# Kernel optimization log

Measured on AMD Instinct MI355X. Metric: run time of the kernel, lower is better.

## Reference

```python
import jax, jax.numpy as jnp
import numpy as np

N = 50000
E_RAND = 800000
F_IN = 128
H = 4          # num_heads
D_HID = 32     # hidden per-head dim
D_OUT = 32     # output per-head dim
NEG_SLOPE_ATTN = 0.2   # DGL GATConv attention leaky_relu
NEG_SLOPE_ACT = 0.01   # F.leaky_relu default activation


def setup_inputs() -> dict:
    key = jax.random.key(0)
    ks = jax.random.split(key, 12)
    x = jax.random.normal(ks[0], (N, F_IN), dtype=jnp.float32)
    src_r = jax.random.randint(ks[1], (E_RAND,), 0, N, dtype=jnp.int32)
    dst_r = jax.random.randint(ks[2], (E_RAND,), 0, N, dtype=jnp.int32)
    loop = jnp.arange(N, dtype=jnp.int32)
    src = jnp.concatenate([src_r, loop])  # add_self_loop
    dst = jnp.concatenate([dst_r, loop])
    sc1 = 1.0 / np.sqrt(F_IN)
    sc2 = 1.0 / np.sqrt(H * D_HID)
    W1 = jax.random.normal(ks[3], (F_IN, H * D_HID), dtype=jnp.float32) * sc1
    al1 = jax.random.normal(ks[4], (H, D_HID), dtype=jnp.float32) * sc1
    ar1 = jax.random.normal(ks[5], (H, D_HID), dtype=jnp.float32) * sc1
    b1 = jnp.zeros((H * D_HID,), dtype=jnp.float32)
    W2 = jax.random.normal(ks[6], (H * D_HID, H * D_OUT), dtype=jnp.float32) * sc2
    al2 = jax.random.normal(ks[7], (H, D_OUT), dtype=jnp.float32) * sc2
    ar2 = jax.random.normal(ks[8], (H, D_OUT), dtype=jnp.float32) * sc2
    b2 = jnp.zeros((H * D_OUT,), dtype=jnp.float32)
    return {"x": x, "src": src, "dst": dst,
            "W1": W1, "al1": al1, "ar1": ar1, "b1": b1,
            "W2": W2, "al2": al2, "ar2": ar2, "b2": b2}


def gat_conv(x, src, dst, W, al, ar, b, act_slope):
    n = x.shape[0]
    h, d = al.shape
    feat = (x @ W).reshape(n, h, d)                 # [N,H,D]
    el = jnp.einsum('nhd,hd->nh', feat, al)         # [N,H]
    er = jnp.einsum('nhd,hd->nh', feat, ar)
    # edge attention score on edge u->v: leaky_relu(el[u] + er[v])
    e = jax.nn.leaky_relu(el[src] + er[dst], NEG_SLOPE_ATTN)  # [E,H]
    # edge softmax over incoming edges of each dst node (self-loops guarantee >=1 edge)
    m = jax.ops.segment_max(e, dst, num_segments=n)           # [N,H]
    ex = jnp.exp(e - m[dst])
    s = jax.ops.segment_sum(ex, dst, num_segments=n)
    a = ex / s[dst]                                           # [E,H]
    # attention-weighted scatter-sum of source features
    out = jax.ops.segment_sum(a[:, :, None] * feat[src], dst, num_segments=n)  # [N,H,D]
    out = out + b.reshape(h, d)
    if act_slope is not None:
        out = jax.nn.leaky_relu(out, act_slope)
    return out.reshape(n, h * d)                    # flatten(1)


def reference(x, src, dst, W1, al1, ar1, b1, W2, al2, ar2, b2):
    h = gat_conv(x, src, dst, W1, al1, ar1, b1, NEG_SLOPE_ACT)
    out = gat_conv(h, src, dst, W2, al2, ar2, b2, None)  # last layer: no activation
    return out
```

## Files before the change

### kernel.cpp

```cpp
#include <hip/hip_runtime.h>
#include <hip/hip_bf16.h>
#include <hip/hip_fp16.h>

#define HEADS 4
#define DHEAD 32
#define FDIM 128
#define BCAP 64
#define RPB 64
#define BINSH 8
#define MAXBINS 256
#define NREP 4
#define WSTRIDE 68

__device__ __forceinline__ void stage_W(const float* __restrict__ W, float* Ws) {
    const float4* Wg = (const float4*)W;
    float4* Wl = (float4*)Ws;
    for (int i = threadIdx.x; i < FDIM * FDIM / 4; i += 256)
        Wl[i] = Wg[i];
}

__device__ __forceinline__ void gemm_core(
    const float* __restrict__ X, const float* __restrict__ al,
    const float* __restrict__ ar, __half* __restrict__ feat,
    float* __restrict__ el, float* __restrict__ er, int n, const float* Ws) {
    int head = __builtin_amdgcn_readfirstlane(threadIdx.x >> 6);
    int lane = threadIdx.x & 63;
    int row = blockIdx.x * RPB + lane;
    bool valid = row < n;
    int cr = valid ? row : (n - 1);
    const float4* xp = (const float4*)(X + (size_t)cr * FDIM);

    const float* wb = Ws + head * DHEAD;

    float acc[32];
#pragma unroll
    for (int j = 0; j < 32; j++) acc[j] = 0.f;

    float4 a = xp[0];
    for (int k4 = 0; k4 < FDIM / 4; k4++) {
        float4 an = (k4 < FDIM / 4 - 1) ? xp[k4 + 1] : a;
#pragma unroll
        for (int kk = 0; kk < 4; kk++) {
            const float4* wr = (const float4*)(wb + (size_t)(k4 * 4 + kk) * FDIM);
            float s = (&a.x)[kk];
#pragma unroll
            for (int j4 = 0; j4 < 8; j4++) {
                float4 wv = wr[j4];
                acc[j4 * 4 + 0] += s * wv.x;
                acc[j4 * 4 + 1] += s * wv.y;
                acc[j4 * 4 + 2] += s * wv.z;
                acc[j4 * 4 + 3] += s * wv.w;
            }
        }
        a = an;
    }

    float elv = 0.f, erv = 0.f;
#pragma unroll
    for (int j = 0; j < 32; j++) {
        elv += acc[j] * al[head * DHEAD + j];
        erv += acc[j] * ar[head * DHEAD + j];
    }
    if (valid) {
        el[(size_t)row * HEADS + head] = elv;
        er[(size_t)row * HEADS + head] = erv;
    }

    if (valid) {
        union { __half2 h2[16]; uint4 u4[4]; } pk;
#pragma unroll
        for (int m = 0; m < 16; m++)
            pk.h2[m] = __floats2half2_rn(acc[2 * m], acc[2 * m + 1]);
        uint4* dstp = (uint4*)(feat + (size_t)row * FDIM + head * DHEAD);
#pragma unroll
        for (int t = 0; t < 4; t++) dstp[t] = pk.u4[t];
    }
}

__global__ __launch_bounds__(256) void k_gemm_l1(
    const float* __restrict__ X, const float* __restrict__ W,
    const float* __restrict__ al, const float* __restrict__ ar,
    __half* __restrict__ feat, float* __restrict__ el, float* __restrict__ er, int n,
    const int* __restrict__ edst, int* __restrict__ bincnt, int E) {
    __shared__ float Ws[FDIM * FDIM];
    int* hist = (int*)Ws;

    for (int i = threadIdx.x; i < MAXBINS; i += 256) hist[i] = 0;
    __syncthreads();
    {
        int nb = gridDim.x;
        int echunk = (E + nb - 1) / nb;
        int e0 = blockIdx.x * echunk;
        int e1 = e0 + echunk; if (e1 > E) e1 = E;
        for (int idx = e0 + threadIdx.x; idx < e1; idx += 256)
            atomicAdd(&hist[__builtin_nontemporal_load(&edst[idx]) >> BINSH], 1);
        __syncthreads();
        int hv = hist[threadIdx.x];
        if (hv) atomicAdd(&bincnt[(blockIdx.x & (NREP - 1)) * MAXBINS + threadIdx.x], hv);
    }
    __syncthreads();

    stage_W(W, Ws);
    __syncthreads();
    gemm_core(X, al, ar, feat, el, er, n, Ws);
}

__global__ __launch_bounds__(256) void k_gemm_l2(
    const float* __restrict__ X, const float* __restrict__ W,
    const float* __restrict__ al, const float* __restrict__ ar,
    __half* __restrict__ feat, float* __restrict__ el, float* __restrict__ er, int n) {
    __shared__ float Ws[FDIM * FDIM];
    stage_W(W, Ws);
    __syncthreads();
    gemm_core(X, al, ar, feat, el, er, n, Ws);
}

__global__ __launch_bounds__(256) void k_p2(
    const int* __restrict__ esrc, const int* __restrict__ edst,
    const int* __restrict__ bincnt, int* __restrict__ cursor,
    uint* __restrict__ ebin, int E, int nbins) {
    __shared__ int sb[MAXBINS];
    __shared__ int lcnt[MAXBINS];
    __shared__ int lbase[MAXBINS];
    int tid = threadIdx.x;
    int v0 = 0;
#pragma unroll
    for (int r = 0; r < NREP; r++) v0 += bincnt[r * MAXBINS + tid];
    sb[tid] = v0;
    lcnt[tid] = 0;
    __syncthreads();
    for (int off = 1; off < MAXBINS; off <<= 1) {
        int t = 0;
        if (tid >= off) t = sb[tid - off];
        __syncthreads();
        if (tid >= off) sb[tid] += t;
        __syncthreads();
    }
    int e0 = blockIdx.x * 2560;
    int e1 = e0 + 2560; if (e1 > E) e1 = E;
    int d[10], s[10], lo[10], bb[10];
    bool v[10];
#pragma unroll
    for (int j = 0; j < 10; j++) {
        int idx = e0 + j * 256 + tid;
        v[j] = idx < e1;
        if (v[j]) {
            d[j] = __builtin_nontemporal_load(&edst[idx]);
            s[j] = __builtin_nontemporal_load(&esrc[idx]);
            bb[j] = d[j] >> BINSH;
            lo[j] = atomicAdd(&lcnt[bb[j]], 1);
        }
    }
    __syncthreads();
    int lc = lcnt[tid];
    if (tid < nbins && lc > 0)
        lbase[tid] = (sb[tid] - v0) + atomicAdd(&cursor[tid], lc);
    __syncthreads();
#pragma unroll
    for (int j = 0; j < 10; j++)
        if (v[j])
            ebin[lbase[bb[j]] + lo[j]] = (uint)(d[j] & 0xffff) | ((uint)s[j] << 16);
}

__global__ __launch_bounds__(256) void k_p3(
    const uint* __restrict__ ebin, const int* __restrict__ bincnt,
    ushort* __restrict__ bucket, int* __restrict__ deg, int n) {
    __shared__ int sb[MAXBINS];
    __shared__ int ldeg[MAXBINS];
    int tid = threadIdx.x;
    int v0 = 0;
#pragma unroll
    for (int r = 0; r < NREP; r++) v0 += bincnt[r * MAXBINS + tid];
    sb[tid] = v0;
    ldeg[tid] = 0;
    __syncthreads();
    for (int off = 1; off < MAXBINS; off <<= 1) {
        int t = 0;
        if (tid >= off) t = sb[tid - off];
        __syncthreads();
        if (tid >= off) sb[tid] += t;
        __syncthreads();
    }
    int bin = blockIdx.x;
    int hi = sb[bin];
    int lo = bin > 0 ? sb[bin - 1] : 0;
    int nb0 = bin << BINSH;
    for (int i = lo + tid; i < hi; i += 256) {
        uint e = ebin[i];
        int dn = (int)(e & 0xffffu);
        int slot = atomicAdd(&ldeg[dn - nb0], 1);
        if (slot < BCAP) bucket[((size_t)dn << 6) + slot] = (ushort)(e >> 16);
    }
    __syncthreads();
    int node = nb0 + tid;
    if (node < n) deg[node] = ldeg[tid];
}

__device__ __forceinline__ void agg_body(
    const ushort* __restrict__ bucket, const int* __restrict__ deg,
    const __half2* __restrict__ feat2h, const float* __restrict__ el,
    const float* __restrict__ er, const float* __restrict__ b,
    float* __restrict__ out, int n, int apply_act) {
    __shared__ float ws_all[4][HEADS * WSTRIDE];
    int wave = threadIdx.x >> 6;
    int node = blockIdx.x * 4 + wave;
    if (node >= n) return;
    node = __builtin_amdgcn_readfirstlane(node);
    int lane = threadIdx.x & 63;
    float* ws = ws_all[wave];

    int cnt = __builtin_amdgcn_readfirstlane(deg[node]);
    if (cnt > BCAP) cnt = BCAP;
    const ushort* bkt = bucket + ((size_t)node << 6);

    {
        int ph = lane >> 4;
        int sl = lane & 15;
        float ern = er[(size_t)node * HEADS + ph];
        int slot[4]; float ev[4];
#pragma unroll
        for (int bb = 0; bb < 4; bb++) {
            slot[bb] = bb * 16 + sl;
            int s = (int)bkt[slot[bb]];
            if (s >= n) s = 0;
            ev[bb] = el[(size_t)s * HEADS + ph];
        }
#pragma unroll
        for (int bb = 0; bb < 4; bb++) {
            float t = ev[bb] + ern;
            t = t > 0.f ? t : 0.2f * t;
            float w = (slot[bb] < cnt) ? __expf(t) : 0.f;
            ws[ph * WSTRIDE + slot[bb]] = w;
        }
    }
    asm volatile("s_waitcnt lgkmcnt(0)" ::: "memory");

    int h = lane >> 4;
    const float2* wsh2 = (const float2*)(ws + h * WSTRIDE);
    const uint* bp32 = (const uint*)bkt;
    float ax = 0.f, ay = 0.f, sw = 0.f;
    int pairs = (cnt + 1) >> 1;
    for (int k0 = 0; k0 < pairs; k0 += 4) {
        uint pk[4];
#pragma unroll
        for (int u = 0; u < 4; u++) {
            int kk = k0 + u;
            pk[u] = __builtin_amdgcn_readfirstlane(kk < pairs ? bp32[kk] : 0u);
        }
        __half2 f[8]; float2 w2[4];
#pragma unroll
        for (int u = 0; u < 4; u++) {
            int s0 = (int)(pk[u] & 0xffffu), s1 = (int)(pk[u] >> 16);
            if (s0 >= n) s0 = 0;
            if (s1 >= n) s1 = 0;
            f[2 * u]     = feat2h[(size_t)s0 * 64 + lane];
            f[2 * u + 1] = feat2h[(size_t)s1 * 64 + lane];
            w2[u] = wsh2[k0 + u];
        }
#pragma unroll
        for (int u = 0; u < 4; u++) {
            float2 f0 = __half22float2(f[2 * u]);
            float2 f1 = __half22float2(f[2 * u + 1]);
            sw += w2[u].x + w2[u].y;
            ax += w2[u].x * f0.x + w2[u].y * f1.x;
            ay += w2[u].x * f0.y + w2[u].y * f1.y;
        }
    }

    float inv = 1.0f / sw;
    float2 bv = ((const float2*)b)[lane];
    float ox = ax * inv + bv.x;
    float oy = ay * inv + bv.y;
    if (apply_act) {
        ox = ox > 0.f ? ox : 0.01f * ox;
        oy = oy > 0.f ? oy : 0.01f * oy;
    }
    float2 o; o.x = ox; o.y = oy;
    ((float2*)out)[(size_t)node * 64 + lane] = o;
}

__global__ __launch_bounds__(256) void k_agg_l1(
    const ushort* __restrict__ bucket, const int* __restrict__ deg,
    const __half2* __restrict__ feat2h, const float* __restrict__ el,
    const float* __restrict__ er, const float* __restrict__ b,
    float* __restrict__ out, int n) {
    agg_body(bucket, deg, feat2h, el, er, b, out, n, 1);
}

__global__ __launch_bounds__(256) void k_agg_l2(
    const ushort* __restrict__ bucket, const int* __restrict__ deg,
    const __half2* __restrict__ feat2h, const float* __restrict__ el,
    const float* __restrict__ er, const float* __restrict__ b,
    float* __restrict__ out, int n) {
    agg_body(bucket, deg, feat2h, el, er, b, out, n, 0);
}


extern "C" void kernel_launch(void* const* d_in, const int* in_sizes, int n_in,
                              void* d_out, int out_size, void* d_ws, size_t ws_size,
                              hipStream_t stream) {
    const float* x   = (const float*)d_in[0];
    const int*   src = (const int*)d_in[1];
    const int*   dst = (const int*)d_in[2];
    const float* W1  = (const float*)d_in[3];
    const float* al1 = (const float*)d_in[4];
    const float* ar1 = (const float*)d_in[5];
    const float* b1  = (const float*)d_in[6];
    const float* W2  = (const float*)d_in[7];
    const float* al2 = (const float*)d_in[8];
    const float* ar2 = (const float*)d_in[9];
    const float* b2  = (const float*)d_in[10];
    int N = in_sizes[0] / FDIM;
    int E = in_sizes[1];
    float* out = (float*)d_out;

    __half* featA   = (__half*)d_ws;
    float*  elb     = (float*)(featA + (size_t)N * FDIM);
    float*  erb     = elb + (size_t)N * HEADS;
    int*    deg     = (int*)(erb + (size_t)N * HEADS);
    int*    bincnt  = deg + N;
    int*    cursor  = bincnt + NREP * MAXBINS;
    ushort* bucket  = (ushort*)(cursor + MAXBINS);
    float*  hbuf    = out;
    uint*   ebin    = (uint*)d_out;

    int gblocks = (N + RPB - 1) / RPB;
    int ablocks = (N + 3) / 4;
    int nbins = (N + (1 << BINSH) - 1) >> BINSH;
    int p2b = (E + 2559) / 2560;

    (void)hipMemsetAsync(bincnt, 0, (NREP + 1) * MAXBINS * sizeof(int), stream);

    k_gemm_l1<<<gblocks, 256, 0, stream>>>(x, W1, al1, ar1, featA, elb, erb, N,
                                           dst, bincnt, E);
    k_p2<<<p2b, 256, 0, stream>>>(src, dst, bincnt, cursor, ebin, E, nbins);
    k_p3<<<nbins, 256, 0, stream>>>(ebin, bincnt, bucket, deg, N);

    k_agg_l1<<<ablocks, 256, 0, stream>>>(bucket, deg, (const __half2*)featA,
                                          elb, erb, b1, hbuf, N);

    k_gemm_l2<<<gblocks, 256, 0, stream>>>(hbuf, W2, al2, ar2, featA, elb, erb, N);
    k_agg_l2<<<ablocks, 256, 0, stream>>>(bucket, deg, (const __half2*)featA,
                                          elb, erb, b2, out, N);
}
```

Measured before the change: 284.0 us.

## Restructure node GEMM into register-blocked tiles with X staged in LDS

The projection GEMM now stages a 64-row X tile in padded shared memory and streams W in four 32-row K-chunks, rather than holding the whole 64KB W in LDS. Each thread computes a 4-row by 8-column register block instead of one row by 32 columns, which raises arithmetic intensity per LDS read. The el/er head dot products are finished with cross-lane shuffle reductions. The intent is to cut the LDS footprint for better occupancy and improve reuse, at the cost of extra barriers per K-chunk and an added shuffle step.

```diff
diff --git a/kernel.cpp b/kernel.cpp
--- a/kernel.cpp
+++ b/kernel.cpp
@@ -7,73 +7,103 @@
 #define FDIM 128
 #define BCAP 64
 #define RPB 64
+#define XP4 33
 #define BINSH 8
 #define MAXBINS 256
 #define NREP 4
 #define WSTRIDE 68
 
-__device__ __forceinline__ void stage_W(const float* __restrict__ W, float* Ws) {
-    const float4* Wg = (const float4*)W;
-    float4* Wl = (float4*)Ws;
-    for (int i = threadIdx.x; i < FDIM * FDIM / 4; i += 256)
-        Wl[i] = Wg[i];
-}
+typedef float nfloat4 __attribute__((ext_vector_type(4)));
 
 __device__ __forceinline__ void gemm_core(
-    const float* __restrict__ X, const float* __restrict__ al,
-    const float* __restrict__ ar, __half* __restrict__ feat,
-    float* __restrict__ el, float* __restrict__ er, int n, const float* Ws) {
+    const float* __restrict__ X, const float* __restrict__ W,
+    const float* __restrict__ al, const float* __restrict__ ar,
+    __half* __restrict__ feat, float* __restrict__ el, float* __restrict__ er,
+    int n, float* Xs , float* Wc ) {
+    int r0 = blockIdx.x * RPB;
+    int rowsLeft = n - r0; if (rowsLeft > RPB) rowsLeft = RPB;
+    {
+        nfloat4* xsw = (nfloat4*)Xs;
+        const nfloat4* Xg = (const nfloat4*)(X + (size_t)r0 * FDIM);
+        for (int i = threadIdx.x; i < RPB * (FDIM / 4); i += 256) {
+            int row = i >> 5, c4 = i & 31;
+            int sr = row < rowsLeft ? row : 0;
+            xsw[row * XP4 + c4] =
+                __builtin_nontemporal_load(&Xg[(size_t)sr * (FDIM / 4) + c4]);
+        }
+    }
+
     int head = __builtin_amdgcn_readfirstlane(threadIdx.x >> 6);
     int lane = threadIdx.x & 63;
-    int row = blockIdx.x * RPB + lane;
-    bool valid = row < n;
-    int cr = valid ? row : (n - 1);
-    const float4* xp = (const float4*)(X + (size_t)cr * FDIM);
-
-    const float* wb = Ws + head * DHEAD;
-
-    float acc[32];
-#pragma unroll
-    for (int j = 0; j < 32; j++) acc[j] = 0.f;
-
-    float4 a = xp[0];
-    for (int k4 = 0; k4 < FDIM / 4; k4++) {
-        float4 an = (k4 < FDIM / 4 - 1) ? xp[k4 + 1] : a;
-#pragma unroll
-        for (int kk = 0; kk < 4; kk++) {
-            const float4* wr = (const float4*)(wb + (size_t)(k4 * 4 + kk) * FDIM);
-            float s = (&a.x)[kk];
-#pragma unroll
-            for (int j4 = 0; j4 < 8; j4++) {
-                float4 wv = wr[j4];
-                acc[j4 * 4 + 0] += s * wv.x;
-                acc[j4 * 4 + 1] += s * wv.y;
-                acc[j4 * 4 + 2] += s * wv.z;
-                acc[j4 * 4 + 3] += s * wv.w;
+    int rg = lane & 15, cg = lane >> 4;
+
+    const float4* Xs4 = (const float4*)Xs;
+    const float4* Wc4 = (const float4*)Wc;
+    const float4* Wg4 = (const float4*)W;
+    float4* Wcw = (float4*)Wc;
+
+    float acc[4][8];
+#pragma unroll
+    for (int m = 0; m < 4; m++)
+#pragma unroll
+        for (int j = 0; j < 8; j++) acc[m][j] = 0.f;
+
+    for (int kc = 0; kc < 4; kc++) {
+        __syncthreads();
+        for (int i = threadIdx.x; i < 1024; i += 256)
+            Wcw[i] = Wg4[kc * 1024 + i];
+        __syncthreads();
+#pragma unroll
+        for (int k4l = 0; k4l < 8; k4l++) {
+            float4 xf[4];
+#pragma unroll
+            for (int m = 0; m < 4; m++)
+                xf[m] = Xs4[(rg + 16 * m) * XP4 + kc * 8 + k4l];
+#pragma unroll
+            for (int kk = 0; kk < 4; kk++) {
+                int wb = (k4l * 4 + kk) * 32 + head * 8 + cg * 2;
+                float4 w0 = Wc4[wb], w1 = Wc4[wb + 1];
+#pragma unroll
+                for (int m = 0; m < 4; m++) {
+                    float s = (&xf[m].x)[kk];
+                    acc[m][0] += s * w0.x; acc[m][1] += s * w0.y;
+                    acc[m][2] += s * w0.z; acc[m][3] += s * w0.w;
+                    acc[m][4] += s * w1.x; acc[m][5] += s * w1.y;
+                    acc[m][6] += s * w1.z; acc[m][7] += s * w1.w;
+                }
             }
         }
-        a = an;
-    }
-
-    float elv = 0.f, erv = 0.f;
-#pragma unroll
-    for (int j = 0; j < 32; j++) {
-        elv += acc[j] * al[head * DHEAD + j];
-        erv += acc[j] * ar[head * DHEAD + j];
-    }
-    if (valid) {
-        el[(size_t)row * HEADS + head] = elv;
-        er[(size_t)row * HEADS + head] = erv;
-    }
-
-    if (valid) {
-        union { __half2 h2[16]; uint4 u4[4]; } pk;
-#pragma unroll
-        for (int m = 0; m < 16; m++)
-            pk.h2[m] = __floats2half2_rn(acc[2 * m], acc[2 * m + 1]);
-        uint4* dstp = (uint4*)(feat + (size_t)row * FDIM + head * DHEAD);
-#pragma unroll
-        for (int t = 0; t < 4; t++) dstp[t] = pk.u4[t];
+    }
+
+    const float4* al4 = (const float4*)al;
+    const float4* ar4 = (const float4*)ar;
+    float4 a0 = al4[head * 8 + cg * 2], a1 = al4[head * 8 + cg * 2 + 1];
+    float4 r0v = ar4[head * 8 + cg * 2], r1v = ar4[head * 8 + cg * 2 + 1];
+#pragma unroll
+    for (int m = 0; m < 4; m++) {
+        float pel = acc[m][0]*a0.x + acc[m][1]*a0.y + acc[m][2]*a0.z + acc[m][3]*a0.w
+                  + acc[m][4]*a1.x + acc[m][5]*a1.y + acc[m][6]*a1.z + acc[m][7]*a1.w;
+        float per = acc[m][0]*r0v.x + acc[m][1]*r0v.y + acc[m][2]*r0v.z + acc[m][3]*r0v.w
+                  + acc[m][4]*r1v.x + acc[m][5]*r1v.y + acc[m][6]*r1v.z + acc[m][7]*r1v.w;
+        pel += __shfl_xor(pel, 16, 64); pel += __shfl_xor(pel, 32, 64);
+        per += __shfl_xor(per, 16, 64); per += __shfl_xor(per, 32, 64);
+        int row = r0 + rg + 16 * m;
+        if (cg == 0 && row < n) {
+            el[(size_t)row * HEADS + head] = pel;
+            er[(size_t)row * HEADS + head] = per;
+        }
+    }
+
+#pragma unroll
+    for (int m = 0; m < 4; m++) {
+        int row = r0 + rg + 16 * m;
+        if (row < n) {
+            union { __half2 h2[4]; uint4 u4; } pk;
+#pragma unroll
+            for (int t = 0; t < 4; t++)
+                pk.h2[t] = __floats2half2_rn(acc[m][2 * t], acc[m][2 * t + 1]);
+            *(uint4*)(feat + (size_t)row * FDIM + head * DHEAD + cg * 8) = pk.u4;
+        }
     }
 }
 
@@ -82,8 +112,9 @@
     const float* __restrict__ al, const float* __restrict__ ar,
     __half* __restrict__ feat, float* __restrict__ el, float* __restrict__ er, int n,
     const int* __restrict__ edst, int* __restrict__ bincnt, int E) {
-    __shared__ float Ws[FDIM * FDIM];
-    int* hist = (int*)Ws;
+    __shared__ float Xs[RPB * XP4 * 4];
+    __shared__ float Wc[32 * FDIM];
+    int* hist = (int*)Xs;
 
     for (int i = threadIdx.x; i < MAXBINS; i += 256) hist[i] = 0;
     __syncthreads();
@@ -100,19 +131,16 @@
     }
     __syncthreads();
 
-    stage_W(W, Ws);
-    __syncthreads();
-    gemm_core(X, al, ar, feat, el, er, n, Ws);
+    gemm_core(X, W, al, ar, feat, el, er, n, Xs, Wc);
 }
 
 __global__ __launch_bounds__(256) void k_gemm_l2(
     const float* __restrict__ X, const float* __restrict__ W,
     const float* __restrict__ al, const float* __restrict__ ar,
     __half* __restrict__ feat, float* __restrict__ el, float* __restrict__ er, int n) {
-    __shared__ float Ws[FDIM * FDIM];
-    stage_W(W, Ws);
-    __syncthreads();
-    gemm_core(X, al, ar, feat, el, er, n, Ws);
+    __shared__ float Xs[RPB * XP4 * 4];
+    __shared__ float Wc[32 * FDIM];
+    gemm_core(X, W, al, ar, feat, el, er, n, Xs, Wc);
 }
 
 __global__ __launch_bounds__(256) void k_p2(
```

Measured after the change: 269.6 us. 1.05x faster.
